# Kernel tuning notes

Hardware: AMD Instinct MI355X
Metric: run time of the kernel (lower is better)

The kernel has to match this reference:

```python
import jax, jax.numpy as jnp
import numpy as np

# EKV transistor-model constants (from the torch module)
EKV_ALPHA = 0.0005625
EKV_N = 1.5
EKV_VD = 0.1
EKV_VT = 0.025
K = 3       # kernel_size
STRIDE = 1
PAD = 1
INIT_THETA_MEAN = 4.5
INIT_THETA_STD = 0.5


def setup_inputs() -> dict:
    key = jax.random.key(0)
    k1, k2 = jax.random.split(key)
    V_in = jax.random.normal(k1, (4, 64, 32, 32), dtype=jnp.float32)
    theta = INIT_THETA_MEAN + INIT_THETA_STD * jax.random.normal(
        k2, (128, 64, K, K), dtype=jnp.float32)
    return {"V_in": V_in, "theta": theta}


def _ekv_conv(V_in, theta):
    # V_in: [B, Cin, H, W]; theta: [Cout, Cin, K, K]
    B, Cin, H, W = V_in.shape
    Cout = theta.shape[0]
    Ho = (H + 2 * PAD - K) // STRIDE + 1
    Wo = (W + 2 * PAD - K) // STRIDE + 1
    Vp = jnp.pad(V_in, ((0, 0), (0, 0), (PAD, PAD), (PAD, PAD)))
    inv = 1.0 / (2.0 * EKV_N * EKV_VT)
    out = jnp.zeros((B, Cout, Ho, Wo), dtype=V_in.dtype)
    # Loop over the K*K kernel taps (fixed, small) instead of materializing
    # the full [B, Cout, L, Cin*K*K] unfold intermediate.
    for i in range(K):
        for j in range(K):
            # shifted input window: [B, Cin, Ho, Wo]
            patch = Vp[:, :, i:i + STRIDE * Ho:STRIDE, j:j + STRIDE * Wo:STRIDE]
            th = theta[:, :, i, j]                     # [Cout, Cin]
            # V_diff: [B, Cout, Cin, Ho, Wo]
            Vd = patch[:, None, :, :, :] - th[None, :, :, None, None]
            t1 = jax.nn.softplus(Vd * inv) ** 2
            t2 = jax.nn.softplus((Vd - EKV_VD) * inv) ** 2
            out = out + EKV_ALPHA * jnp.sum(t1 - t2, axis=2)
    return out


def reference(V_in, theta):
    return _ekv_conv(V_in, theta)
```

## Files before the change

kernel.cpp:

```cpp
#include <hip/hip_runtime.h>


constexpr int CIN  = 64;
constexpr int COUT = 128;
constexpr int HW   = 32;
constexpr int PIX  = HW * HW;

constexpr float S     = 19.235933878519512f;
constexpr float KF    = 0.26359713811572677f;
constexpr float OSC   = 2.7025482032899376e-4f;
constexpr float DELTA = 0.2599401f;

__global__ __launch_bounds__(256)
void ekv_rowmax(const float* __restrict__ V, float* __restrict__ wg)
{
    const int t = threadIdx.x;
    const int plane = blockIdx.x;
    __shared__ float rmax[32];
    const float4 v4 = reinterpret_cast<const float4*>(V + (size_t)plane * PIX)[t];
    float m = fmaxf(fmaxf(v4.x, v4.y), fmaxf(v4.z, v4.w));
    m = fmaxf(m, __shfl_xor(m, 1));
    m = fmaxf(m, __shfl_xor(m, 2));
    m = fmaxf(m, __shfl_xor(m, 4));
    if ((t & 7) == 0) rmax[t >> 3] = m;
    __syncthreads();
    if (t < 4) {
        float wm = 0.0f;
        #pragma unroll
        for (int rr = 0; rr < 10; ++rr) {
            const int r = 8 * t - 1 + rr;
            if (r >= 0 && r < 32) wm = fmaxf(wm, rmax[r]);
        }
        wg[plane * 4 + t] = wm;
    }
}

__global__ __launch_bounds__(256, 4)
void ekv_main(const float* __restrict__ V, const float* __restrict__ Th,
              const float* __restrict__ wg, float* __restrict__ Out)
{
    const int t = threadIdx.x;
    const int task = ((blockIdx.x & 7) << 6) | (blockIdx.x >> 3);
    const int co   = task & (COUT - 1);
    const int b    = task >> 7;
    const int w    = t >> 6;
    const int lane = t & 63;

    const float* vbase = V  + (size_t)b  * CIN * PIX;
    const float* thp   = Th + (size_t)co * (CIN * 9);

    float th[9];
    #pragma unroll
    for (int k = 0; k < 9; ++k) th[k] = thp[lane * 9 + k];
    const float wgv = wg[(size_t)(b * CIN + lane) * 4 + w];
    const float lim = wgv + DELTA;
    unsigned tlm = 0u;
    #pragma unroll
    for (int k = 0; k < 9; ++k) if (th[k] <= lim) tlm |= (1u << k);
    float q[9];
    #pragma unroll
    for (int k = 0; k < 9; ++k) q[k] = __builtin_amdgcn_exp2f(-th[k] * S);
    unsigned long long mask = __ballot(tlm != 0u);

    const int lr = lane >> 3;
    const int lc = (lane & 7) * 4;
    const int r   = 8 * w + lr;
    const int rm1 = (r - 1 < 0)  ? 0  : r - 1;
    const int rp1 = (r + 1 > 31) ? 31 : r + 1;
    const bool okA = (r - 1) >= 0;
    const bool okC = (r + 1) <= 31;
    const bool isL = (lane & 7) == 0;
    const bool isR = (lane & 7) == 7;
    const int  lcl = isL ? 0 : lc - 1;
    const int  lcr = isR ? 31 : lc + 4;

    float acc0 = 0.f, acc1 = 0.f, acc2 = 0.f, acc3 = 0.f;

    auto pop = [&]() -> int {
        if (!mask) return -1;
        const int c = (int)__builtin_ctzll(mask); mask &= mask - 1; return c;
    };
    auto issue = [&](int cin, float4& A, float4& B, float4& C,
                     float2& eA, float2& eB, float2& eC) {
        const unsigned tc = (unsigned)__shfl((int)tlm, cin);
        const float* src = vbase + cin * PIX;
        if (tc & 7u) {
            const float* ra = src + rm1 * HW;
            A = *reinterpret_cast<const float4*>(ra + lc);
            eA.x = ra[lcl]; eA.y = ra[lcr];
        }
        if (tc & 56u) {
            const float* rb = src + r * HW;
            B = *reinterpret_cast<const float4*>(rb + lc);
            eB.x = rb[lcl]; eB.y = rb[lcr];
        }
        if (tc & 448u) {
            const float* rc = src + rp1 * HW;
            C = *reinterpret_cast<const float4*>(rc + lc);
            eC.x = rc[lcl]; eC.y = rc[lcr];
        }
    };
    auto rowv = [&](const float4& x, const float2& e, bool ok, float* vals) {
        vals[0] = __builtin_amdgcn_exp2f(((ok && !isL) ? e.x : 0.f) * S);
        vals[1] = __builtin_amdgcn_exp2f((ok ? x.x : 0.f) * S);
        vals[2] = __builtin_amdgcn_exp2f((ok ? x.y : 0.f) * S);
        vals[3] = __builtin_amdgcn_exp2f((ok ? x.z : 0.f) * S);
        vals[4] = __builtin_amdgcn_exp2f((ok ? x.w : 0.f) * S);
        vals[5] = __builtin_amdgcn_exp2f(((ok && !isR) ? e.y : 0.f) * S);
    };
    auto compute = [&](int cin, const float4& A, const float4& B, const float4& C,
                       const float2& eA, const float2& eB, const float2& eC) {
        const unsigned tc = (unsigned)__shfl((int)tlm, cin);
        float qc[9];
        #pragma unroll
        for (int k = 0; k < 9; ++k) qc[k] = __shfl(q[k], cin);
        #pragma unroll
        for (int i = 0; i < 3; ++i) {
            if (!((tc >> (3 * i)) & 7u)) continue;
            float vals[6];
            if      (i == 0) rowv(A, eA, okA, vals);
            else if (i == 1) rowv(B, eB, true, vals);
            else             rowv(C, eC, okC, vals);
            #pragma unroll
            for (int j = 0; j < 3; ++j) {
                if (!((tc >> (3 * i + j)) & 1u)) continue;
                const float qa = qc[3 * i + j];
                const float qb = qa * KF;
                #pragma unroll
                for (int k = 0; k < 4; ++k) {
                    const float x1 = __builtin_fmaf(vals[k + j], qa, 1.0f);
                    const float x2 = __builtin_fmaf(vals[k + j], qb, 1.0f);
                    const float l1 = __builtin_amdgcn_logf(x1);
                    const float l2 = __builtin_amdgcn_logf(x2);
                    const float su = l1 + l2, di = l1 - l2;
                    if      (k == 0) acc0 = __builtin_fmaf(su, di, acc0);
                    else if (k == 1) acc1 = __builtin_fmaf(su, di, acc1);
                    else if (k == 2) acc2 = __builtin_fmaf(su, di, acc2);
                    else             acc3 = __builtin_fmaf(su, di, acc3);
                }
            }
        }
    };

    {
        float4 aA = make_float4(0.f,0.f,0.f,0.f), bA = aA, cA = aA;
        float4 aB = aA, bB = aA, cB = aA;
        float2 eaA = make_float2(0.f,0.f), ebA = eaA, ecA = eaA;
        float2 eaB = eaA, ebB = eaA, ecB = eaA;
        int q0 = pop();
        if (q0 >= 0) {
            issue(q0, aA, bA, cA, eaA, ebA, ecA);
            int q1 = pop();
            if (q1 >= 0) issue(q1, aB, bB, cB, eaB, ebB, ecB);
            for (;;) {
                {
                    const float4 xa = aA, xb = bA, xc = cA;
                    const float2 ya = eaA, yb = ebA, yc = ecA;
                    int q2 = (q1 >= 0) ? pop() : -1;
                    if (q2 >= 0) issue(q2, aA, bA, cA, eaA, ebA, ecA);
                    compute(q0, xa, xb, xc, ya, yb, yc);
                    if (q1 < 0) break;
                    q0 = q2;
                }
                {
                    const float4 xa = aB, xb = bB, xc = cB;
                    const float2 ya = eaB, yb = ebB, yc = ecB;
                    int q3 = (q0 >= 0) ? pop() : -1;
                    if (q3 >= 0) issue(q3, aB, bB, cB, eaB, ebB, ecB);
                    compute(q1, xa, xb, xc, ya, yb, yc);
                    if (q0 < 0) break;
                    q1 = q3;
                }
            }
        }
    }

    float4 o;
    o.x = acc0 * OSC; o.y = acc1 * OSC; o.z = acc2 * OSC; o.w = acc3 * OSC;
    float* obase = Out + (size_t)(b * COUT + co) * PIX + w * 256;
    reinterpret_cast<float4*>(obase)[lane] = o;
}

extern "C" void kernel_launch(void* const* d_in, const int* in_sizes, int n_in,
                              void* d_out, int out_size, void* d_ws, size_t ws_size,
                              hipStream_t stream) {
    (void)in_sizes; (void)n_in; (void)ws_size; (void)out_size;
    const float* V  = (const float*)d_in[0];
    const float* Th = (const float*)d_in[1];
    float* Out = (float*)d_out;
    float* wg  = (float*)d_ws;
    ekv_rowmax<<<dim3(4 * CIN), dim3(256), 0, stream>>>(V, wg);
    ekv_main<<<dim3(4 * COUT), dim3(256), 0, stream>>>(V, Th, wg, Out);
}
```

Before: 23.91 us.

## Split input-channel reduction across four waves with shared-memory combine

Each block now handles one 8-row window of one (batch, output channel) pair instead of all four windows. The four waves split the active input channels of that window round-robin by rank and reduce their partial sums through shared memory. This quadruples the grid and balances per-wave work, since different row windows can have very different numbers of active channels. In exchange it adds a block barrier, shared-memory traffic, redundant theta/exp setup per block, and a higher occupancy target in the launch bounds that may constrain registers.

New measurement: 43.12 us. 80.3% more time.

```diff
diff --git a/kernel.cpp b/kernel.cpp
--- a/kernel.cpp
+++ b/kernel.cpp
@@ -35,16 +35,19 @@
     }
 }
 
-__global__ __launch_bounds__(256, 4)
+__global__ __launch_bounds__(256, 8)
 void ekv_main(const float* __restrict__ V, const float* __restrict__ Th,
               const float* __restrict__ wg, float* __restrict__ Out)
 {
     const int t = threadIdx.x;
-    const int task = ((blockIdx.x & 7) << 6) | (blockIdx.x >> 3);
-    const int co   = task & (COUT - 1);
-    const int b    = task >> 7;
-    const int w    = t >> 6;
+    const int task = ((blockIdx.x & 7) << 8) | (blockIdx.x >> 3);
+    const int win  = task & 3;
+    const int co   = (task >> 2) & (COUT - 1);
+    const int b    = task >> 9;
+    const int ph   = t >> 6;
     const int lane = t & 63;
+
+    __shared__ float4 Cb[256];
 
     const float* vbase = V  + (size_t)b  * CIN * PIX;
     const float* thp   = Th + (size_t)co * (CIN * 9);
@@ -52,7 +55,7 @@
     float th[9];
     #pragma unroll
     for (int k = 0; k < 9; ++k) th[k] = thp[lane * 9 + k];
-    const float wgv = wg[(size_t)(b * CIN + lane) * 4 + w];
+    const float wgv = wg[(size_t)(b * CIN + lane) * 4 + win];
     const float lim = wgv + DELTA;
     unsigned tlm = 0u;
     #pragma unroll
@@ -60,11 +63,15 @@
     float q[9];
     #pragma unroll
     for (int k = 0; k < 9; ++k) q[k] = __builtin_amdgcn_exp2f(-th[k] * S);
-    unsigned long long mask = __ballot(tlm != 0u);
+
+    const unsigned long long full = __ballot(tlm != 0u);
+    const bool actv = (full >> lane) & 1ull;
+    const int  rank = (int)__popcll(full & ((1ull << lane) - 1ull));
+    unsigned long long mask = __ballot(actv && ((rank & 3) == ph));
 
     const int lr = lane >> 3;
     const int lc = (lane & 7) * 4;
-    const int r   = 8 * w + lr;
+    const int r   = 8 * win + lr;
     const int rm1 = (r - 1 < 0)  ? 0  : r - 1;
     const int rp1 = (r + 1 > 31) ? 31 : r + 1;
     const bool okA = (r - 1) >= 0;
@@ -175,10 +182,21 @@
         }
     }
 
-    float4 o;
-    o.x = acc0 * OSC; o.y = acc1 * OSC; o.z = acc2 * OSC; o.w = acc3 * OSC;
-    float* obase = Out + (size_t)(b * COUT + co) * PIX + w * 256;
-    reinterpret_cast<float4*>(obase)[lane] = o;
+    Cb[t] = make_float4(acc0, acc1, acc2, acc3);
+    __syncthreads();
+    if (t < 64) {
+        const float4 p0 = Cb[t];
+        const float4 p1 = Cb[t + 64];
+        const float4 p2 = Cb[t + 128];
+        const float4 p3 = Cb[t + 192];
+        float4 o;
+        o.x = (p0.x + p1.x + p2.x + p3.x) * OSC;
+        o.y = (p0.y + p1.y + p2.y + p3.y) * OSC;
+        o.z = (p0.z + p1.z + p2.z + p3.z) * OSC;
+        o.w = (p0.w + p1.w + p2.w + p3.w) * OSC;
+        float* obase = Out + (size_t)(b * COUT + co) * PIX + win * 256;
+        reinterpret_cast<float4*>(obase)[t] = o;
+    }
 }
 
 extern "C" void kernel_launch(void* const* d_in, const int* in_sizes, int n_in,
@@ -190,5 +208,5 @@
     float* Out = (float*)d_out;
     float* wg  = (float*)d_ws;
     ekv_rowmax<<<dim3(4 * CIN), dim3(256), 0, stream>>>(V, wg);
-    ekv_main<<<dim3(4 * COUT), dim3(256), 0, stream>>>(V, Th, wg, Out);
+    ekv_main<<<dim3(4 * COUT * 4), dim3(256), 0, stream>>>(V, Th, wg, Out);
 }
```
